# Performance work log

Hardware: AMD Instinct MI355X
Metric: run time of the kernel (lower is better)

The kernel has to match this reference:

```python
import jax, jax.numpy as jnp
import numpy as np

L, B, T, D, H, A, F, V, BIAS_DIM, E = 6, 16, 512, 512, 8, 64, 2048, 10000, 4, 200000
LN_EPS = 1e-3  # keras LayerNormalization default


def positional_encoding(d, max_len):
    pos = np.arange(max_len, dtype=np.float32)[:, None]
    i = np.arange(d, dtype=np.float32)[None, :]
    angle = pos / np.power(10000.0, (2.0 * np.floor(i / 2.0)) / d)
    pe = np.where((np.arange(d) % 2) == 0, np.sin(angle), np.cos(angle))
    return jnp.asarray(pe, jnp.float32)


def layer_norm(x, g, b):
    mu = jnp.mean(x, -1, keepdims=True)
    var = jnp.mean(jnp.square(x - mu), -1, keepdims=True)
    return (x - mu) * jax.lax.rsqrt(var + LN_EPS) * g + b


def attention(x, masks, bias_idx, Wq, Wk, Wv, Wo, be, bs):
    q = jnp.einsum('btd,dha->btha', x, Wq)
    k = jnp.einsum('btd,dha->btha', x, Wk)
    v = jnp.einsum('btd,dha->btha', x, Wv)
    alpha = jnp.einsum('bkha,bqha->bhqk', k, q)
    # sparse edge bias: scalar per edge = bias_embs[type] @ bias_scalar
    ev = (be[bias_idx[:, 0]] @ bs)[:, 0]                      # [E]
    dense = jnp.zeros((x.shape[0], x.shape[1], x.shape[1]), x.dtype)
    dense = dense.at[bias_idx[:, 1], bias_idx[:, 2], bias_idx[:, 3]].add(ev)  # scatter_nd semantics (add)
    ksum = jnp.sum(k, -1)                                     # [B,T,H]
    alpha = alpha + jnp.einsum('bqk,bkh->bhqk', dense, ksum)
    alpha = alpha * jax.lax.rsqrt(jnp.float32(A))
    alpha = alpha * masks + (1.0 - jnp.ceil(masks)) * jnp.finfo(jnp.float32).min
    alpha = jax.nn.softmax(alpha, -1)
    ctx = jnp.einsum('bhqk,bkha->bqha', alpha, v)
    return jnp.einsum('btha,had->btd', ctx, Wo)


def setup_inputs() -> dict:
    key = jax.random.key(0)
    ks = jax.random.split(key, 24)
    tokens = jax.random.randint(ks[0], (B, T), 0, V, dtype=jnp.int32)
    masks = jnp.ones((B, 1, T, T), jnp.float32)
    ab = jnp.stack([
        jax.random.randint(ks[1], (E,), 0, BIAS_DIM, dtype=jnp.int32),
        jax.random.randint(ks[2], (E,), 0, B, dtype=jnp.int32),
        jax.random.randint(ks[3], (E,), 0, T, dtype=jnp.int32),
        jax.random.randint(ks[4], (E,), 0, T, dtype=jnp.int32)], axis=1)
    s = 0.03
    return {
        'tokens': tokens, 'masks': masks, 'attention_bias': ab,
        'embed': jax.random.normal(ks[5], (V, D)) * (D ** -0.5),
        'Wq': jax.random.normal(ks[6], (L, D, H, A)) * s,
        'Wk': jax.random.normal(ks[7], (L, D, H, A)) * s,
        'Wv': jax.random.normal(ks[8], (L, D, H, A)) * s,
        'Wo': jax.random.normal(ks[9], (L, H, A, D)) * s,
        'be': jax.random.normal(ks[10], (L, BIAS_DIM, A)) * s,
        'bs': jax.random.normal(ks[11], (L, A, 1)) * s,
        'ln_g': jnp.ones((L, 2, D)), 'ln_b': jnp.zeros((L, 2, D)),
        'ff1_w': jax.random.normal(ks[12], (L, D, F)) * s,
        'ff1_b': jnp.zeros((L, F)),
        'ff2_w': jax.random.normal(ks[13], (L, F, D)) * s,
        'ff2_b': jnp.zeros((L, D)),
        'lnout_g': jnp.ones((D,)), 'lnout_b': jnp.zeros((D,)),
    }


def reference(tokens, masks, attention_bias, embed, Wq, Wk, Wv, Wo, be, bs,
              ln_g, ln_b, ff1_w, ff1_b, ff2_w, ff2_b, lnout_g, lnout_b):
    pos_enc = positional_encoding(D, 5000)
    x = embed[tokens] * jnp.sqrt(jnp.float32(D)) + pos_enc[:T]
    for l in range(L):
        h = layer_norm(x, ln_g[l, 0], ln_b[l, 0])
        x = x + attention(h, masks, attention_bias, Wq[l], Wk[l], Wv[l], Wo[l], be[l], bs[l])
        h = layer_norm(x, ln_g[l, 1], ln_b[l, 1])
        x = x + jax.nn.relu(h @ ff1_w[l] + ff1_b[l]) @ ff2_w[l] + ff2_b[l]
    return layer_norm(x, lnout_g, lnout_b)
```

## Files before the change

kernel.cpp:

```cpp
#include <hip/hip_runtime.h>
#include <hip/hip_bf16.h>

#define LNUM 6
#define BB 16
#define TT 512
#define DD 512
#define HH 8
#define AA 64
#define FFD 2048
#define EE 200000
#define BIASDIM 4
#define ATT_NEG (-3.402823466e38f)

typedef __bf16 bf16_t;
typedef __attribute__((ext_vector_type(8))) __bf16 bf16x8;
typedef __attribute__((ext_vector_type(4))) float f32x4;

typedef __attribute__((address_space(3))) void lds_void;
typedef const __attribute__((address_space(1))) void glb_void;

__device__ __forceinline__ void async_load16(const bf16_t* g, bf16_t* l) {
    __builtin_amdgcn_global_load_lds((glb_void*)g, (lds_void*)l, 16, 0, 0);
}

__global__ __launch_bounds__(256) void embed_pe_kernel(
    const int* __restrict__ tokens, const float* __restrict__ embed,
    float* __restrict__ x)
{
    int idx = blockIdx.x * 256 + threadIdx.x;
    int d  = idx & (DD - 1);
    int bt = idx >> 9;
    int t  = bt & (TT - 1);
    int tok = tokens[bt];
    float e = embed[(long long)tok * DD + d] * 22.62741699796952f;
    float p = (float)(2 * (d >> 1)) * (1.0f / (float)DD);
    float denom = exp2f(p * 13.287712379549449f);
    float angle = (float)t / denom;
    float pe = (d & 1) ? cosf(angle) : sinf(angle);
    x[idx] = e + pe;
}

template <typename TO>
__global__ __launch_bounds__(256) void ln_kernel(
    const float* __restrict__ x, TO* __restrict__ y,
    const float* __restrict__ g, const float* __restrict__ b)
{
    long long row = blockIdx.x;
    const float* xr = x + row * DD;
    int tid = threadIdx.x;
    float v0 = xr[tid], v1 = xr[tid + 256];
    float s = v0 + v1, sq = v0 * v0 + v1 * v1;
#pragma unroll
    for (int o = 32; o > 0; o >>= 1) {
        s  += __shfl_down(s, o);
        sq += __shfl_down(sq, o);
    }
    __shared__ float ss[4], sq4[4];
    if ((tid & 63) == 0) { ss[tid >> 6] = s; sq4[tid >> 6] = sq; }
    __syncthreads();
    float st  = ss[0] + ss[1] + ss[2] + ss[3];
    float sqt = sq4[0] + sq4[1] + sq4[2] + sq4[3];
    float mean = st * (1.0f / DD);
    float var  = sqt * (1.0f / DD) - mean * mean;
    float inv  = rsqrtf(var + 1e-3f);
    y[row * DD + tid]       = (TO)((v0 - mean) * inv * g[tid]       + b[tid]);
    y[row * DD + tid + 256] = (TO)((v1 - mean) * inv * g[tid + 256] + b[tid + 256]);
}

__global__ __launch_bounds__(256) void ksum_kernel(
    const bf16_t* __restrict__ k, float* __restrict__ ks)
{
    int idx = blockIdx.x * 256 + threadIdx.x;
    long long base = (long long)idx * AA;
    float s = 0.f;
#pragma unroll
    for (int a = 0; a < AA; a++) s += (float)k[base + a];
    ks[idx] = s;
}

__global__ __launch_bounds__(256) void bias_scatter_kernel(
    const int* __restrict__ ab, const float* __restrict__ be,
    const float* __restrict__ bs, float* __restrict__ dense)
{
    __shared__ float ev[BIASDIM];
    int tid = threadIdx.x;
    if (tid < BIASDIM) {
        float s = 0.f;
        for (int a = 0; a < AA; a++) s += be[tid * AA + a] * bs[a];
        ev[tid] = s;
    }
    __syncthreads();
    int e = blockIdx.x * 256 + tid;
    if (e < EE) {
        int ty = ab[e * 4 + 0];
        int b  = ab[e * 4 + 1];
        int q  = ab[e * 4 + 2];
        int kk = ab[e * 4 + 3];
        atomicAdd(&dense[((long long)b * TT + q) * TT + kk], ev[ty]);
    }
}

__global__ __launch_bounds__(256) void wconv_kernel(
    const float* __restrict__ in, bf16_t* __restrict__ out, int R, int Cc)
{
    __shared__ bf16_t tile[64][65];
    int c0 = blockIdx.x * 64, r0 = blockIdx.y * 64;
    int tid = threadIdx.x;
#pragma unroll
    for (int i = 0; i < 16; i++) {
        int idx = tid + i * 256; int r = idx >> 6, c = idx & 63;
        tile[c][r] = (bf16_t)in[(long long)(r0 + r) * Cc + c0 + c];
    }
    __syncthreads();
#pragma unroll
    for (int i = 0; i < 16; i++) {
        int idx = tid + i * 256; int rr = idx >> 6, cc = idx & 63;
        out[(long long)(c0 + rr) * R + r0 + cc] = tile[rr][cc];
    }
}

struct Ptr4 { const float* p[4]; };

__global__ __launch_bounds__(256) void wconv4_kernel(Ptr4 srcs, bf16_t* __restrict__ out)
{
    __shared__ bf16_t tile[64][65];
    int z = blockIdx.z;
    const float* in = srcs.p[z];
    bf16_t* o = out + (long long)z * DD * DD;
    int c0 = blockIdx.x * 64, r0 = blockIdx.y * 64;
    int tid = threadIdx.x;
#pragma unroll
    for (int i = 0; i < 16; i++) {
        int idx = tid + i * 256; int r = idx >> 6, c = idx & 63;
        tile[c][r] = (bf16_t)in[(long long)(r0 + r) * DD + c0 + c];
    }
    __syncthreads();
#pragma unroll
    for (int i = 0; i < 16; i++) {
        int idx = tid + i * 256; int rr = idx >> 6, cc = idx & 63;
        o[(long long)(c0 + rr) * DD + r0 + cc] = tile[rr][cc];
    }
}

__global__ __launch_bounds__(256) void vtrans_kernel(
    const bf16_t* __restrict__ v, bf16_t* __restrict__ vT)
{
    __shared__ bf16_t tile[64][65];
    int bh = blockIdx.y; int b = bh >> 3, h = bh & 7;
    int t0 = blockIdx.x * 64;
    int tid = threadIdx.x;
#pragma unroll
    for (int i = 0; i < 16; i++) {
        int idx = tid + i * 256; int r = idx >> 6, c = idx & 63;
        tile[c][r] = v[((long long)(b * TT + t0 + r) * HH + h) * AA + c];
    }
    __syncthreads();
#pragma unroll
    for (int i = 0; i < 16; i++) {
        int idx = tid + i * 256; int a = idx >> 6, t2 = idx & 63;
        vT[(((long long)b * HH + h) * AA + a) * TT + t0 + t2] = tile[a][t2];
    }
}

__global__ __launch_bounds__(256) void fused_attn_kernel(
    const bf16_t* __restrict__ qg, const bf16_t* __restrict__ kg,
    const bf16_t* __restrict__ vT, const float* __restrict__ dense,
    const float* __restrict__ ksum, const float* __restrict__ masks,
    bf16_t* __restrict__ ctx)
{
    __shared__ __align__(16) bf16_t Ks[64 * 64];
    __shared__ __align__(16) bf16_t Vs[64 * 64];
    __shared__ __align__(16) bf16_t Plds[4 * 16 * 88];

    int tid = threadIdx.x;
    int wave = tid >> 6, lane = tid & 63;
    int row16 = lane & 15, quad = lane >> 4;
    int bh = blockIdx.y; int b = bh >> 3, h = bh & 7;
    int qw = blockIdx.x * 64 + wave * 16;

    bf16x8 qf[2];
    {
        const bf16_t* qp = qg + (((long long)b * TT + qw + row16) * HH + h) * AA + quad * 8;
        qf[0] = *(const bf16x8*)(qp);
        qf[1] = *(const bf16x8*)(qp + 32);
    }

    f32x4 o[4] = {};
    float m_r[4], l_r[4];
#pragma unroll
    for (int r = 0; r < 4; r++) { m_r[r] = -3.0e38f; l_r[r] = 0.f; }

    bf16_t* Pw = Plds + wave * 16 * 88;
    const float* dbase = dense + (long long)b * TT * TT;
    const float* mbase = masks + (long long)b * TT * TT;

    for (int kt = 0; kt < 8; kt++) {
        int t0 = kt * 64;
#pragma unroll
        for (int p = tid; p < 512; p += 256) {
            int r = p >> 3, s = p & 7, c = s ^ (r & 7);
            async_load16(kg + (((long long)b * TT + t0 + r) * HH + h) * AA + c * 8,
                         Ks + p * 8);
        }
#pragma unroll
        for (int p = tid; p < 512; p += 256) {
            int r = p >> 3, s = p & 7, c = s ^ (r & 7);
            async_load16(vT + ((long long)bh * AA + r) * TT + t0 + c * 8,
                         Vs + p * 8);
        }
        __syncthreads();

        f32x4 s4[4] = {};
#pragma unroll
        for (int n = 0; n < 4; n++) {
            int row = n * 16 + row16;
            int sw = row & 7;
            bf16x8 kf0 = *(const bf16x8*)(Ks + row * 64 + ((quad ^ sw) * 8));
            bf16x8 kf1 = *(const bf16x8*)(Ks + row * 64 + (((quad + 4) ^ sw) * 8));
            s4[n] = __builtin_amdgcn_mfma_f32_16x16x32_bf16(qf[0], kf0, s4[n], 0, 0, 0);
            s4[n] = __builtin_amdgcn_mfma_f32_16x16x32_bf16(qf[1], kf1, s4[n], 0, 0, 0);
        }

        float val[4][4];
#pragma unroll
        for (int n = 0; n < 4; n++) {
            int ktok = t0 + n * 16 + row16;
            float ksv = ksum[((long long)b * TT + ktok) * HH + h];
#pragma unroll
            for (int r = 0; r < 4; r++) {
                int qgl = qw + quad * 4 + r;
                float d  = dbase[(long long)qgl * TT + ktok];
                float mk = mbase[(long long)qgl * TT + ktok];
                float vv = 0.125f * fmaf(d, ksv, s4[n][r]);
                val[n][r] = vv * mk + (1.0f - ceilf(mk)) * ATT_NEG;
            }
        }

        float scl[4];
#pragma unroll
        for (int r = 0; r < 4; r++) {
            float mx = fmaxf(fmaxf(val[0][r], val[1][r]), fmaxf(val[2][r], val[3][r]));
#pragma unroll
            for (int off = 1; off < 16; off <<= 1) mx = fmaxf(mx, __shfl_xor(mx, off));
            float mnew = fmaxf(m_r[r], mx);
            float sc = __expf(m_r[r] - mnew);
            float ps = 0.f;
#pragma unroll
            for (int n = 0; n < 4; n++) {
                float p = __expf(val[n][r] - mnew);
                val[n][r] = p;
                ps += p;
            }
#pragma unroll
            for (int off = 1; off < 16; off <<= 1) ps += __shfl_xor(ps, off);
            l_r[r] = l_r[r] * sc + ps;
            m_r[r] = mnew;
            scl[r] = sc;
        }
#pragma unroll
        for (int j = 0; j < 4; j++)
#pragma unroll
            for (int r = 0; r < 4; r++) o[j][r] *= scl[r];

#pragma unroll
        for (int n = 0; n < 4; n++)
#pragma unroll
            for (int r = 0; r < 4; r++)
                Pw[(quad * 4 + r) * 88 + n * 16 + row16] = (bf16_t)val[n][r];
        asm volatile("s_waitcnt lgkmcnt(0)" ::: "memory");

        bf16x8 pa0 = *(const bf16x8*)(Pw + row16 * 88 + quad * 8);
        bf16x8 pa1 = *(const bf16x8*)(Pw + row16 * 88 + 32 + quad * 8);
#pragma unroll
        for (int j = 0; j < 4; j++) {
            int row = j * 16 + row16;
            int sw = row & 7;
            bf16x8 vb0 = *(const bf16x8*)(Vs + row * 64 + ((quad ^ sw) * 8));
            bf16x8 vb1 = *(const bf16x8*)(Vs + row * 64 + (((quad + 4) ^ sw) * 8));
            o[j] = __builtin_amdgcn_mfma_f32_16x16x32_bf16(pa0, vb0, o[j], 0, 0, 0);
            o[j] = __builtin_amdgcn_mfma_f32_16x16x32_bf16(pa1, vb1, o[j], 0, 0, 0);
        }
        __syncthreads();
    }

#pragma unroll
    for (int r = 0; r < 4; r++) {
        float invl = 1.0f / l_r[r];
        int qgl = qw + quad * 4 + r;
        bf16_t* cp = ctx + (((long long)b * TT + qgl) * HH + h) * AA;
#pragma unroll
        for (int j = 0; j < 4; j++)
            cp[j * 16 + row16] = (bf16_t)(o[j][r] * invl);
    }
}

template <int BM, int BN, typename TC>
__global__ __launch_bounds__((BM / 64) * (BN / 64) * 64) void gemm_mfma(
    const bf16_t* __restrict__ Ag, const bf16_t* __restrict__ Bg, TC* __restrict__ Cg,
    int K, int lda, int ldb, int ldc,
    const float* __restrict__ bias, int accum, int relu)
{
    constexpr int WN = BN / 64;
    constexpr int NT = (BM / 64) * (BN / 64) * 64;
    __shared__ __align__(16) bf16_t As[BM * 32];
    __shared__ __align__(16) bf16_t Bs[BN * 32];

    int tid = threadIdx.x;
    int wave = tid >> 6, lane = tid & 63;
    int wm = (wave / WN) * 64, wn = (wave % WN) * 64;
    int m0 = blockIdx.x * BM, n0 = blockIdx.y * BN;
    int row16 = lane & 15, quad = lane >> 4;

    f32x4 acc[4][4] = {};

    for (int k0 = 0; k0 < K; k0 += 32) {
#pragma unroll
        for (int p = tid; p < BM * 4; p += NT) {
            int r = p >> 2, c = p & 3;
            async_load16(Ag + (long long)(m0 + r) * lda + k0 + c * 8, As + p * 8);
        }
#pragma unroll
        for (int p = tid; p < BN * 4; p += NT) {
            int r = p >> 2, c = p & 3;
            async_load16(Bg + (long long)(n0 + r) * ldb + k0 + c * 8, Bs + p * 8);
        }
        __syncthreads();
        bf16x8 af[4], bfr[4];
#pragma unroll
        for (int i = 0; i < 4; i++)
            af[i] = *(const bf16x8*)(As + (wm + i * 16 + row16) * 32 + quad * 8);
#pragma unroll
        for (int j = 0; j < 4; j++)
            bfr[j] = *(const bf16x8*)(Bs + (wn + j * 16 + row16) * 32 + quad * 8);
#pragma unroll
        for (int i = 0; i < 4; i++)
#pragma unroll
            for (int j = 0; j < 4; j++)
                acc[i][j] = __builtin_amdgcn_mfma_f32_16x16x32_bf16(
                    af[i], bfr[j], acc[i][j], 0, 0, 0);
        __syncthreads();
    }

#pragma unroll
    for (int i = 0; i < 4; i++) {
#pragma unroll
        for (int j = 0; j < 4; j++) {
#pragma unroll
            for (int r = 0; r < 4; r++) {
                int m = m0 + wm + i * 16 + quad * 4 + r;
                int n = n0 + wn + j * 16 + row16;
                float vv = acc[i][j][r];
                if (bias) vv += bias[n];
                if (accum) vv += (float)Cg[(long long)m * ldc + n];
                if (relu) vv = fmaxf(vv, 0.f);
                Cg[(long long)m * ldc + n] = (TC)vv;
            }
        }
    }
}

extern "C" void kernel_launch(void* const* d_in, const int* in_sizes, int n_in,
                              void* d_out, int out_size, void* d_ws, size_t ws_size,
                              hipStream_t stream)
{
    const int*   tokens = (const int*)d_in[0];
    const float* masks  = (const float*)d_in[1];
    const int*   ab     = (const int*)d_in[2];
    const float* embed  = (const float*)d_in[3];
    const float* Wq     = (const float*)d_in[4];
    const float* Wk     = (const float*)d_in[5];
    const float* Wv     = (const float*)d_in[6];
    const float* Wo     = (const float*)d_in[7];
    const float* be     = (const float*)d_in[8];
    const float* bs     = (const float*)d_in[9];
    const float* ln_g   = (const float*)d_in[10];
    const float* ln_b   = (const float*)d_in[11];
    const float* ff1w   = (const float*)d_in[12];
    const float* ff1b   = (const float*)d_in[13];
    const float* ff2w   = (const float*)d_in[14];
    const float* ff2b   = (const float*)d_in[15];
    const float* lng    = (const float*)d_in[16];
    const float* lnb    = (const float*)d_in[17];
    float* out = (float*)d_out;

    const long long NX = (long long)BB * TT * DD;
    float* x     = (float*)d_ws;
    float* dense = x + NX;
    float* ks    = dense + (long long)BB * TT * TT;
    bf16_t* h_bf = (bf16_t*)(ks + (long long)BB * TT * HH);
    bf16_t* q    = h_bf + NX;
    bf16_t* k    = q + NX;
    bf16_t* v    = k + NX;
    bf16_t* vT   = v + NX;
    bf16_t* wqT  = vT + NX;
    bf16_t* wkT  = wqT + (long long)DD * DD;
    bf16_t* wvT  = wkT + (long long)DD * DD;
    bf16_t* woT  = wvT + (long long)DD * DD;
    bf16_t* ff1T = woT + (long long)DD * DD;
    bf16_t* ff2T = ff1T + (long long)DD * FFD;
    bf16_t* ffm  = ff2T + (long long)FFD * DD;

    embed_pe_kernel<<<dim3(NX / 256), dim3(256), 0, stream>>>(tokens, embed, x);

    for (int l = 0; l < LNUM; l++) {
        Ptr4 p4;
        p4.p[0] = Wq + (long long)l * DD * HH * AA;
        p4.p[1] = Wk + (long long)l * DD * HH * AA;
        p4.p[2] = Wv + (long long)l * DD * HH * AA;
        p4.p[3] = Wo + (long long)l * HH * AA * DD;
        wconv4_kernel<<<dim3(8, 8, 4), dim3(256), 0, stream>>>(p4, wqT);
        wconv_kernel<<<dim3(FFD / 64, DD / 64, 1), dim3(256), 0, stream>>>(
            ff1w + (long long)l * DD * FFD, ff1T, DD, FFD);
        wconv_kernel<<<dim3(DD / 64, FFD / 64, 1), dim3(256), 0, stream>>>(
            ff2w + (long long)l * FFD * DD, ff2T, FFD, DD);

        const float* ff1b_l = ff1b + (long long)l * FFD;
        const float* ff2b_l = ff2b + (long long)l * DD;

        ln_kernel<bf16_t><<<dim3(BB * TT), dim3(256), 0, stream>>>(
            x, h_bf, ln_g + (l * 2 + 0) * DD, ln_b + (l * 2 + 0) * DD);

        gemm_mfma<128, 128, bf16_t><<<dim3(64, 4, 1), dim3(256), 0, stream>>>(
            h_bf, wqT, q, 512, 512, 512, 512, nullptr, 0, 0);
        gemm_mfma<128, 128, bf16_t><<<dim3(64, 4, 1), dim3(256), 0, stream>>>(
            h_bf, wkT, k, 512, 512, 512, 512, nullptr, 0, 0);
        gemm_mfma<128, 128, bf16_t><<<dim3(64, 4, 1), dim3(256), 0, stream>>>(
            h_bf, wvT, v, 512, 512, 512, 512, nullptr, 0, 0);

        vtrans_kernel<<<dim3(8, BB * HH), dim3(256), 0, stream>>>(v, vT);
        ksum_kernel<<<dim3(BB * TT * HH / 256), dim3(256), 0, stream>>>(k, ks);

        hipMemsetAsync(dense, 0, sizeof(float) * (size_t)BB * TT * TT, stream);
        bias_scatter_kernel<<<dim3((EE + 255) / 256), dim3(256), 0, stream>>>(
            ab, be + (long long)l * BIASDIM * AA, bs + (long long)l * AA, dense);

        fused_attn_kernel<<<dim3(TT / 64, BB * HH), dim3(256), 0, stream>>>(
            q, k, vT, dense, ks, masks, h_bf);

        gemm_mfma<128, 128, float><<<dim3(64, 4, 1), dim3(256), 0, stream>>>(
            h_bf, woT, x, 512, 512, 512, 512, nullptr, 1, 0);

        ln_kernel<bf16_t><<<dim3(BB * TT), dim3(256), 0, stream>>>(
            x, h_bf, ln_g + (l * 2 + 1) * DD, ln_b + (l * 2 + 1) * DD);

        gemm_mfma<128, 128, bf16_t><<<dim3(64, 16, 1), dim3(256), 0, stream>>>(
            h_bf, ff1T, ffm, 512, 512, 512, 2048, ff1b_l, 0, 1);

        gemm_mfma<128, 128, float><<<dim3(64, 4, 1), dim3(256), 0, stream>>>(
            ffm, ff2T, x, 2048, 2048, 2048, 512, ff2b_l, 1, 0);
    }

    ln_kernel<float><<<dim3(BB * TT), dim3(256), 0, stream>>>(x, out, lng, lnb);
}
```

Before: 1.824 ms.

## Batch QKV GEMMs via grid z and split-K the Wo/FF2 GEMMs with atomics

The three Q/K/V projection GEMMs become one launch that uses blockIdx.z to select the weight and output slices. The residual-accumulating Wo and FF2 GEMMs switch to split-K (2 and 4 slices) and add their partial sums into x with float atomicAdd. The aim is to cut launch count and fill the GPU with more blocks on the small-N GEMMs. The cost is atomic traffic on the output and a summation order that can differ from run to run.

```diff
diff --git a/kernel.cpp b/kernel.cpp
--- a/kernel.cpp
+++ b/kernel.cpp
@@ -294,16 +294,21 @@
     }
 }
 
-template <int BM, int BN, typename TC>
+template <int BM, int BN, typename TC, bool ATOMIC>
 __global__ __launch_bounds__((BM / 64) * (BN / 64) * 64) void gemm_mfma(
     const bf16_t* __restrict__ Ag, const bf16_t* __restrict__ Bg, TC* __restrict__ Cg,
     int K, int lda, int ldb, int ldc,
+    long long sAz, long long sBz, long long sCz,
     const float* __restrict__ bias, int accum, int relu)
 {
     constexpr int WN = BN / 64;
     constexpr int NT = (BM / 64) * (BN / 64) * 64;
     __shared__ __align__(16) bf16_t As[BM * 32];
     __shared__ __align__(16) bf16_t Bs[BN * 32];
+
+    int z = blockIdx.z;
+    Ag += z * sAz; Bg += z * sBz; Cg += z * sCz;
+    if (ATOMIC && z != 0) bias = nullptr;
 
     int tid = threadIdx.x;
     int wave = tid >> 6, lane = tid & 63;
@@ -351,9 +356,13 @@
                 int n = n0 + wn + j * 16 + row16;
                 float vv = acc[i][j][r];
                 if (bias) vv += bias[n];
-                if (accum) vv += (float)Cg[(long long)m * ldc + n];
-                if (relu) vv = fmaxf(vv, 0.f);
-                Cg[(long long)m * ldc + n] = (TC)vv;
+                if (ATOMIC) {
+                    atomicAdd((float*)&Cg[(long long)m * ldc + n], vv);
+                } else {
+                    if (accum) vv += (float)Cg[(long long)m * ldc + n];
+                    if (relu) vv = fmaxf(vv, 0.f);
+                    Cg[(long long)m * ldc + n] = (TC)vv;
+                }
             }
         }
     }
@@ -420,12 +429,9 @@
         ln_kernel<bf16_t><<<dim3(BB * TT), dim3(256), 0, stream>>>(
             x, h_bf, ln_g + (l * 2 + 0) * DD, ln_b + (l * 2 + 0) * DD);
 
-        gemm_mfma<128, 128, bf16_t><<<dim3(64, 4, 1), dim3(256), 0, stream>>>(
-            h_bf, wqT, q, 512, 512, 512, 512, nullptr, 0, 0);
-        gemm_mfma<128, 128, bf16_t><<<dim3(64, 4, 1), dim3(256), 0, stream>>>(
-            h_bf, wkT, k, 512, 512, 512, 512, nullptr, 0, 0);
-        gemm_mfma<128, 128, bf16_t><<<dim3(64, 4, 1), dim3(256), 0, stream>>>(
-            h_bf, wvT, v, 512, 512, 512, 512, nullptr, 0, 0);
+        gemm_mfma<128, 128, bf16_t, false><<<dim3(64, 4, 3), dim3(256), 0, stream>>>(
+            h_bf, wqT, q, 512, 512, 512, 512,
+            0LL, (long long)DD * DD, NX, nullptr, 0, 0);
 
         vtrans_kernel<<<dim3(8, BB * HH), dim3(256), 0, stream>>>(v, vT);
         ksum_kernel<<<dim3(BB * TT * HH / 256), dim3(256), 0, stream>>>(k, ks);
@@ -437,17 +443,19 @@
         fused_attn_kernel<<<dim3(TT / 64, BB * HH), dim3(256), 0, stream>>>(
             q, k, vT, dense, ks, masks, h_bf);
 
-        gemm_mfma<128, 128, float><<<dim3(64, 4, 1), dim3(256), 0, stream>>>(
-            h_bf, woT, x, 512, 512, 512, 512, nullptr, 1, 0);
+        gemm_mfma<128, 128, float, true><<<dim3(64, 4, 2), dim3(256), 0, stream>>>(
+            h_bf, woT, x, 256, 512, 512, 512,
+            256LL, 256LL, 0LL, nullptr, 0, 0);
 
         ln_kernel<bf16_t><<<dim3(BB * TT), dim3(256), 0, stream>>>(
             x, h_bf, ln_g + (l * 2 + 1) * DD, ln_b + (l * 2 + 1) * DD);
 
-        gemm_mfma<128, 128, bf16_t><<<dim3(64, 16, 1), dim3(256), 0, stream>>>(
-            h_bf, ff1T, ffm, 512, 512, 512, 2048, ff1b_l, 0, 1);
-
-        gemm_mfma<128, 128, float><<<dim3(64, 4, 1), dim3(256), 0, stream>>>(
-            ffm, ff2T, x, 2048, 2048, 2048, 512, ff2b_l, 1, 0);
+        gemm_mfma<128, 128, bf16_t, false><<<dim3(64, 16, 1), dim3(256), 0, stream>>>(
+            h_bf, ff1T, ffm, 512, 512, 512, 2048, 0LL, 0LL, 0LL, ff1b_l, 0, 1);
+
+        gemm_mfma<128, 128, float, true><<<dim3(64, 4, 4), dim3(256), 0, stream>>>(
+            ffm, ff2T, x, 512, 2048, 2048, 512,
+            512LL, 512LL, 0LL, ff2b_l, 0, 0);
     }
 
     ln_kernel<float><<<dim3(BB * TT), dim3(256), 0, stream>>>(x, out, lng, lnb);
```

Result: faster. 1.764 ms (-3.3%).
